# Kernel tuning notes

Hardware: AMD Instinct MI355X
Metric: run time of the kernel (lower is better)

The kernel has to match this reference:

```python
import jax, jax.numpy as jnp
import numpy as np

B, N, D, H, DFF = 2, 2048, 1024, 16, 4096
HD = D // H
L = 3
WINDOWS = (256, 64, 16)   # sliding-window size per hierarchy level
LEVEL_SCALE = 16          # pos_l = token_idx // LEVEL_SCALE**l
EPS = 1e-5
NEG = -1e9


def setup_inputs() -> dict:
    key = jax.random.key(0)
    ks = jax.random.split(key, 16)
    s = 0.02
    x = jax.random.normal(ks[0], (B, N, D), dtype=jnp.float32)
    idx = jnp.arange(N, dtype=jnp.int32)
    positions = jnp.stack([idx // (LEVEL_SCALE ** l) for l in range(L)], axis=0)  # [L, N]
    return {
        "x": x,
        "positions": positions,
        "w_qkv": jax.random.normal(ks[1], (D, 3 * D), dtype=jnp.float32) * s,
        "b_qkv": jnp.zeros((3 * D,), dtype=jnp.float32),
        "w_out": jax.random.normal(ks[2], (D, D), dtype=jnp.float32) * s,
        "b_out": jnp.zeros((D,), dtype=jnp.float32),
        "w_ff1": jax.random.normal(ks[3], (D, DFF), dtype=jnp.float32) * s,
        "b_ff1": jnp.zeros((DFF,), dtype=jnp.float32),
        "w_ff2": jax.random.normal(ks[4], (DFF, D), dtype=jnp.float32) * s,
        "b_ff2": jnp.zeros((D,), dtype=jnp.float32),
        "g1": jnp.ones((D,), dtype=jnp.float32),
        "beta1": jnp.zeros((D,), dtype=jnp.float32),
        "g2": jnp.ones((D,), dtype=jnp.float32),
        "beta2": jnp.zeros((D,), dtype=jnp.float32),
    }


def _layernorm(x, g, b):
    m = jnp.mean(x, axis=-1, keepdims=True)
    v = jnp.var(x, axis=-1, keepdims=True)
    return (x - m) * jax.lax.rsqrt(v + EPS) * g + b


def _mlswa_mask(positions):
    # union over levels of per-level sliding windows: |pos_l[i]-pos_l[j]| < w_l
    allowed = jnp.zeros((N, N), dtype=bool)
    for l, w in enumerate(WINDOWS):
        p = positions[l]
        allowed = allowed | (jnp.abs(p[:, None] - p[None, :]) < w)
    return allowed  # [N, N]


def reference(x, positions, w_qkv, b_qkv, w_out, b_out,
              w_ff1, b_ff1, w_ff2, b_ff2, g1, beta1, g2, beta2):
    residual = x
    xn = _layernorm(x, g1, beta1)
    qkv = xn @ w_qkv + b_qkv                       # [B, N, 3D]
    qkv = qkv.reshape(B, N, 3, H, HD)
    q, k, v = qkv[:, :, 0], qkv[:, :, 1], qkv[:, :, 2]  # [B, N, H, HD]

    scale = 1.0 / np.sqrt(HD)
    scores = jnp.einsum('bihd,bjhd->bhij', q, k) * scale  # [B, H, N, N]
    allowed = _mlswa_mask(positions)
    scores = jnp.where(allowed[None, None], scores, NEG)
    attn = jax.nn.softmax(scores, axis=-1)
    out = jnp.einsum('bhij,bjhd->bihd', attn, v).reshape(B, N, D)
    out = out @ w_out + b_out
    x = residual + out

    residual = x
    xn = _layernorm(x, g2, beta2)
    ff = jax.nn.gelu(xn @ w_ff1 + b_ff1, approximate=False) @ w_ff2 + b_ff2
    return residual + ff
```

## Files before the change

kernel.cpp:

```cpp
#include <hip/hip_runtime.h>
#include <cstdint>
#include <cstddef>


using u16 = unsigned short;
using u32 = unsigned int;

typedef __attribute__((ext_vector_type(8)))  short bf16x8;
typedef __attribute__((ext_vector_type(4)))  float f32x4;
typedef __attribute__((ext_vector_type(16))) float f32x16;

#define DEV __device__ __forceinline__

DEV u16 f2bf(float f) {
  u32 u = __builtin_bit_cast(u32, f);
  u32 r = (u + 0x7FFFu + ((u >> 16) & 1u)) >> 16;
  return (u16)r;
}
DEV float bf2f(u16 u) { return __builtin_bit_cast(float, (u32)u << 16); }
DEV u32 pk2(float a, float b) { return (u32)f2bf(a) | ((u32)f2bf(b) << 16); }
DEV u32 cvtpk(float lo, float hi) {
  u32 r;
  asm("v_cvt_pk_bf16_f32 %0, %1, %2" : "=v"(r) : "v"(lo), "v"(hi));
  return r;
}
DEV float fexp2(float x) { return __builtin_amdgcn_exp2f(x); }

DEV void gload_lds16(const void* g, void* lds) {
  __builtin_amdgcn_global_load_lds(
      (const __attribute__((address_space(1))) u32*)g,
      (__attribute__((address_space(3))) u32*)lds, 16, 0, 0);
}

DEV float fast_gelu(float x) {
  float u = x * fmaf(0.035677408137f, x * x, 0.7978845608f);
  u = fminf(fmaxf(u, -15.0f), 15.0f);
  float e = fexp2(u * 2.885390081777927f);
  return x * e * __builtin_amdgcn_rcpf(e + 1.0f);
}

__global__ __launch_bounds__(256) void k_transpose_bf16(const float* __restrict__ in,
                                                        u16* __restrict__ out, int R, int C) {
  __shared__ float ts[32][33];
  int n0 = blockIdx.x * 32, r0 = blockIdx.y * 32;
  int t = threadIdx.x;
  int c = t & 31, r = t >> 5;
#pragma unroll
  for (int j = 0; j < 4; ++j)
    ts[r + 8 * j][c] = in[(size_t)(r0 + r + 8 * j) * C + n0 + c];
  __syncthreads();
#pragma unroll
  for (int j = 0; j < 4; ++j)
    out[(size_t)(n0 + r + 8 * j) * R + r0 + c] = f2bf(ts[c][r + 8 * j]);
}

__global__ __launch_bounds__(256) void k_layernorm(const float* __restrict__ x,
                                                   const float* __restrict__ g,
                                                   const float* __restrict__ be,
                                                   u16* __restrict__ o) {
  int row = blockIdx.x;
  int t = threadIdx.x;
  const float* xr = x + (size_t)row * 1024;
  f32x4 v = *(const f32x4*)(xr + t * 4);
  float s = v[0] + v[1] + v[2] + v[3];
  float s2 = v[0] * v[0] + v[1] * v[1] + v[2] * v[2] + v[3] * v[3];
#pragma unroll
  for (int off = 1; off < 64; off <<= 1) {
    s += __shfl_xor(s, off);
    s2 += __shfl_xor(s2, off);
  }
  __shared__ float red[8];
  if ((t & 63) == 0) { red[t >> 6] = s; red[4 + (t >> 6)] = s2; }
  __syncthreads();
  s = red[0] + red[1] + red[2] + red[3];
  s2 = red[4] + red[5] + red[6] + red[7];
  float mean = s * (1.0f / 1024.0f);
  float var = fmaxf(s2 * (1.0f / 1024.0f) - mean * mean, 0.0f);
  float rstd = rsqrtf(var + 1e-5f);
  f32x4 gg = *(const f32x4*)(g + t * 4);
  f32x4 bb = *(const f32x4*)(be + t * 4);
  uint2 ww;
  ww.x = pk2((v[0] - mean) * rstd * gg[0] + bb[0], (v[1] - mean) * rstd * gg[1] + bb[1]);
  ww.y = pk2((v[2] - mean) * rstd * gg[2] + bb[2], (v[3] - mean) * rstd * gg[3] + bb[3]);
  *(uint2*)(o + (size_t)row * 1024 + t * 4) = ww;
}

template <int MODE, int SPLIT, int DBUF>
__global__ __launch_bounds__(SPLIT * 256) void k_gemm(
    const u16* __restrict__ A, const u16* __restrict__ Bt, int K, int NC,
    const float* __restrict__ bias, const float* __restrict__ resid,
    void* __restrict__ o0, void* __restrict__ o1, void* __restrict__ o2) {
  __shared__ u16 tiles[SPLIT][1 + DBUF][2][128 * 64];
  const int lane = threadIdx.x & 63, wave = threadIdx.x >> 6;
  const int group = (SPLIT >= 2) ? (wave >> 2) : 0;
  const int wv = wave & 3;
  const int nwg = gridDim.x * gridDim.y;
  const int id = blockIdx.y * gridDim.x + blockIdx.x;
  const int wg = (id & 7) * (nwg >> 3) + (id >> 3);
  const int tN = (wg % gridDim.x) * 128, tM = (wg / gridDim.x) * 128;
  const int wm = (wv >> 1) * 64, wn = (wv & 1) * 64;
  const int lm = lane & 15, lh = lane >> 4;
  const int K2 = K / SPLIT;
  const int kbase = group * K2;
  f32x4 acc[4][4] = {};

  auto STAGE = [&](int k0, int buf) {
#pragma unroll
    for (int i = 0; i < 4; ++i) {
      int seg = i * 4 + wv;
      int li = seg * 64 + lane;
      int m = li >> 3, ch = li & 7;
      gload_lds16(A + (size_t)(tM + m) * K + kbase + k0 + ((ch ^ (m & 7)) << 3),
                  (void*)(tiles[group][buf][0] + seg * 512));
      gload_lds16(Bt + (size_t)(tN + m) * K + kbase + k0 + ((ch ^ (m & 7)) << 3),
                  (void*)(tiles[group][buf][1] + seg * 512));
    }
  };

  auto COMPUTE = [&](int buf) {
#pragma unroll
    for (int s = 0; s < 2; ++s) {
      bf16x8 af[4], bfr[4];
#pragma unroll
      for (int i = 0; i < 4; ++i) {
        int m = wm + i * 16 + lm;
        af[i] = *(const bf16x8*)((const char*)tiles[group][buf][0] + m * 128 +
                                 (((s * 4 + lh) ^ (m & 7)) << 4));
      }
#pragma unroll
      for (int j = 0; j < 4; ++j) {
        int n = wn + j * 16 + lm;
        bfr[j] = *(const bf16x8*)((const char*)tiles[group][buf][1] + n * 128 +
                                  (((s * 4 + lh) ^ (n & 7)) << 4));
      }
#pragma unroll
      for (int i = 0; i < 4; ++i)
#pragma unroll
        for (int j = 0; j < 4; ++j)
          acc[i][j] = __builtin_amdgcn_mfma_f32_16x16x32_bf16(af[i], bfr[j], acc[i][j], 0, 0, 0);
    }
  };

  const int nk = K2 >> 6;
  if constexpr (DBUF == 1) {
    STAGE(0, 0);
    for (int t = 0; t < nk; ++t) {
      const int cur = t & 1;
      if (t + 1 < nk) {
        STAGE((t + 1) << 6, cur ^ 1);
        asm volatile("s_waitcnt vmcnt(8)" ::: "memory");
      } else {
        asm volatile("s_waitcnt vmcnt(0)" ::: "memory");
      }
      __builtin_amdgcn_s_barrier();
      COMPUTE(cur);
      __builtin_amdgcn_s_barrier();
    }
  } else {
    for (int t = 0; t < nk; ++t) {
      __syncthreads();
      STAGE(t << 6, 0);
      __syncthreads();
      COMPUTE(0);
    }
  }

  auto dumpacc = [&](float* c) {
#pragma unroll
    for (int i = 0; i < 4; ++i)
#pragma unroll
      for (int j = 0; j < 4; ++j)
        *(f32x4*)&c[(i * 4 + j) * 1024 + wv * 256 + lane * 4] = acc[i][j];
  };
  auto addacc = [&](const float* c) {
#pragma unroll
    for (int i = 0; i < 4; ++i)
#pragma unroll
      for (int j = 0; j < 4; ++j) {
        f32x4 o4 = *(const f32x4*)&c[(i * 4 + j) * 1024 + wv * 256 + lane * 4];
#pragma unroll
        for (int r = 0; r < 4; ++r) acc[i][j][r] += o4[r];
      }
  };

  if constexpr (SPLIT == 4) {
    float* cA = (float*)&tiles[0][0][0][0];
    float* cB = (float*)&tiles[2][0][0][0];
    __syncthreads();
    if (group == 1) dumpacc(cA);
    if (group == 3) dumpacc(cB);
    __syncthreads();
    if (group == 0) addacc(cA);
    if (group == 2) addacc(cB);
    __syncthreads();
    if (group == 2) dumpacc(cA);
    __syncthreads();
    if (group == 0) { addacc(cA); dumpacc(cB); }
    __syncthreads();
    {
      const int i = group;
#pragma unroll
      for (int j = 0; j < 4; ++j) {
        int gn = tN + wn + j * 16 + lm;
        int gm0 = tM + wm + i * 16 + lh * 4;
        f32x4 v4 = *(const f32x4*)&cB[(i * 4 + j) * 1024 + wv * 256 + lane * 4];
        float bv = bias[gn];
#pragma unroll
        for (int r = 0; r < 4; ++r)
          ((float*)o0)[(size_t)(gm0 + r) * NC + gn] =
              v4[r] + bv + resid[(size_t)(gm0 + r) * NC + gn];
      }
    }
    return;
  }

  if constexpr (SPLIT == 2) {
    float* comb = (float*)tiles;
    __syncthreads();
    if (group == 1) dumpacc(comb);
    __syncthreads();
    if (group == 1) return;
    addacc(comb);
  }

#pragma unroll
  for (int i = 0; i < 4; ++i) {
#pragma unroll
    for (int j = 0; j < 4; ++j) {
      int gn = tN + wn + j * 16 + lm;
      int gm0 = tM + wm + i * 16 + lh * 4;
      float vals[4];
#pragma unroll
      for (int r = 0; r < 4; ++r) vals[r] = acc[i][j][r] + bias[gn];
      if constexpr (MODE == 0) {
        int which = gn >> 10, h = (gn >> 6) & 15, d = gn & 63;
        int b = gm0 >> 11, nn0 = gm0 & 2047;
        if (which == 2) {
          uint2 w2;
          w2.x = pk2(vals[0], vals[1]);
          w2.y = pk2(vals[2], vals[3]);
          *(uint2*)((u16*)o2 + ((size_t)(b * 16 + h) * 64 + d) * 2048 + nn0) = w2;
        } else {
          u16* dst = which == 0 ? (u16*)o0 : (u16*)o1;
          float sc = which == 0 ? 0.18033688011112042f : 1.0f;
#pragma unroll
          for (int r = 0; r < 4; ++r)
            dst[(((size_t)(b * 16 + h)) * 2048 + nn0 + r) * 64 + d] = f2bf(vals[r] * sc);
        }
      } else if constexpr (MODE == 2) {
#pragma unroll
        for (int r = 0; r < 4; ++r)
          ((u16*)o0)[(size_t)(gm0 + r) * NC + gn] = f2bf(fast_gelu(vals[r]));
      } else {
#pragma unroll
        for (int r = 0; r < 4; ++r)
          ((float*)o0)[(size_t)(gm0 + r) * NC + gn] =
              vals[r] + resid[(size_t)(gm0 + r) * NC + gn];
      }
    }
  }
}

__global__ __launch_bounds__(256) void k_attn(const u16* __restrict__ q,
                                              const u16* __restrict__ k,
                                              const u16* __restrict__ vt,
                                              u16* __restrict__ o) {
  __shared__ u16 KT[2][4096];
  __shared__ u16 VT[2][4096];
  const int tid = threadIdx.x;
  const int lane = tid & 63, wave = tid >> 6;
  const int ql = lane & 31, hi = lane >> 5;
  const int id = blockIdx.y * 16 + blockIdx.x;
  const int wg = (id & 7) * 64 + (id >> 3);
  const int qb = wg & 15, bh = wg >> 4;
  const int q0 = qb * 128 + wave * 32;

  const u16* qp = q + ((size_t)bh * 2048 + q0 + ql) * 64 + hi * 8;
  bf16x8 qf[4];
#pragma unroll
  for (int dc = 0; dc < 4; ++dc) qf[dc] = *(const bf16x8*)(qp + dc * 16);

  const u16* kst = k + (size_t)bh * 2048 * 64;
  const u16* vst = vt + (size_t)bh * 64 * 2048;

  f32x16 ot0 = {0, 0, 0, 0, 0, 0, 0, 0, 0, 0, 0, 0, 0, 0, 0, 0};
  f32x16 ot1 = ot0;
  f32x16 ot2 = ot0;
  const bf16x8 ones1 = {16256, 16256, 16256, 16256, 16256, 16256, 16256, 16256};

  u32 koffA[4], koffB[4], voffA[4], voffB[4];
#pragma unroll
  for (int dc = 0; dc < 4; ++dc) {
    u32 sw = (((u32)((dc << 1) | hi) ^ (ql & 7)) << 3);
    koffA[dc] = (ql << 6) + sw;
    koffB[dc] = ((32 + ql) << 6) + sw;
  }
#pragma unroll
  for (int kc = 0; kc < 2; ++kc)
#pragma unroll
    for (int dh = 0; dh < 2; ++dh) {
      u32 rb = ((u32)((dh << 5) + ql) << 6);
      voffA[kc * 2 + dh] = rb + ((((kc << 1) + hi) ^ (ql & 7)) << 3);
      voffB[kc * 2 + dh] = rb + (((4 + (kc << 1) + hi) ^ (ql & 7)) << 3);
    }

  auto STAGE = [&](int tl, int b) {
    int kb = tl << 6;
#pragma unroll
    for (int i = 0; i < 2; ++i) {
      int seg = i * 4 + wave;
      int li = seg * 64 + lane;
      int row = li >> 3, ch = li & 7;
      int sw = (ch ^ (row & 7)) << 3;
      gload_lds16(kst + (size_t)(kb + row) * 64 + sw, (void*)&KT[b][seg * 512]);
      gload_lds16(vst + (size_t)row * 2048 + kb + sw, (void*)&VT[b][seg * 512]);
    }
  };

  auto COMPUTE = [&](const u16* KTb, const u16* VTb) {
    f32x16 st0 = {0, 0, 0, 0, 0, 0, 0, 0, 0, 0, 0, 0, 0, 0, 0, 0};
    f32x16 st1 = st0;
    bf16x8 kfa[4], kfb[4];
#pragma unroll
    for (int dc = 0; dc < 4; ++dc) {
      kfa[dc] = *(const bf16x8*)(KTb + koffA[dc]);
      kfb[dc] = *(const bf16x8*)(KTb + koffB[dc]);
    }
    __builtin_amdgcn_s_setprio(1);
#pragma unroll
    for (int dc = 0; dc < 4; ++dc) {
      st0 = __builtin_amdgcn_mfma_f32_32x32x16_bf16(kfa[dc], qf[dc], st0, 0, 0, 0);
      st1 = __builtin_amdgcn_mfma_f32_32x32x16_bf16(kfb[dc], qf[dc], st1, 0, 0, 0);
    }
    __builtin_amdgcn_s_setprio(0);
    bf16x8 vf0[4], vf1[4];
#pragma unroll
    for (int i = 0; i < 4; ++i) {
      vf0[i] = *(const bf16x8*)(VTb + voffA[i]);
      vf1[i] = *(const bf16x8*)(VTb + voffB[i]);
    }
    float p0[16], p1v[16];
#pragma unroll
    for (int r = 0; r < 16; ++r) {
      p0[r] = fexp2(st0[r]);
      p1v[r] = fexp2(st1[r]);
    }
    __builtin_amdgcn_s_setprio(1);
#pragma unroll
    for (int kc = 0; kc < 2; ++kc) {
      u32 x0 = cvtpk(p0[kc * 8 + 0], p0[kc * 8 + 1]), x1 = cvtpk(p0[kc * 8 + 2], p0[kc * 8 + 3]);
      u32 y0 = cvtpk(p0[kc * 8 + 4], p0[kc * 8 + 5]), y1 = cvtpk(p0[kc * 8 + 6], p0[kc * 8 + 7]);
      asm("v_permlane32_swap_b32 %0, %1" : "+v"(x0), "+v"(y0));
      asm("v_permlane32_swap_b32 %0, %1" : "+v"(x1), "+v"(y1));
      union { u32 u[4]; bf16x8 v8; } pf;
      pf.u[0] = x0; pf.u[1] = x1; pf.u[2] = y0; pf.u[3] = y1;
      ot0 = __builtin_amdgcn_mfma_f32_32x32x16_bf16(vf0[kc * 2 + 0], pf.v8, ot0, 0, 0, 0);
      ot1 = __builtin_amdgcn_mfma_f32_32x32x16_bf16(vf0[kc * 2 + 1], pf.v8, ot1, 0, 0, 0);
      ot2 = __builtin_amdgcn_mfma_f32_32x32x16_bf16(ones1, pf.v8, ot2, 0, 0, 0);
    }
#pragma unroll
    for (int kc = 0; kc < 2; ++kc) {
      u32 x0 = cvtpk(p1v[kc * 8 + 0], p1v[kc * 8 + 1]), x1 = cvtpk(p1v[kc * 8 + 2], p1v[kc * 8 + 3]);
      u32 y0 = cvtpk(p1v[kc * 8 + 4], p1v[kc * 8 + 5]), y1 = cvtpk(p1v[kc * 8 + 6], p1v[kc * 8 + 7]);
      asm("v_permlane32_swap_b32 %0, %1" : "+v"(x0), "+v"(y0));
      asm("v_permlane32_swap_b32 %0, %1" : "+v"(x1), "+v"(y1));
      union { u32 u[4]; bf16x8 v8; } pf;
      pf.u[0] = x0; pf.u[1] = x1; pf.u[2] = y0; pf.u[3] = y1;
      ot0 = __builtin_amdgcn_mfma_f32_32x32x16_bf16(vf1[kc * 2 + 0], pf.v8, ot0, 0, 0, 0);
      ot1 = __builtin_amdgcn_mfma_f32_32x32x16_bf16(vf1[kc * 2 + 1], pf.v8, ot1, 0, 0, 0);
      ot2 = __builtin_amdgcn_mfma_f32_32x32x16_bf16(ones1, pf.v8, ot2, 0, 0, 0);
    }
    __builtin_amdgcn_s_setprio(0);
  };

  STAGE(0, 0);
  __syncthreads();

#pragma unroll 1
  for (int t2 = 0; t2 < 16; ++t2) {
    const int tlA = t2 * 2;
    STAGE(tlA + 1, 1);
    COMPUTE(KT[0], VT[0]);
    __syncthreads();
    if (t2 < 15) STAGE(tlA + 2, 0);
    COMPUTE(KT[1], VT[1]);
    __syncthreads();
  }

  float inv = 1.0f / ot2[0];
  int b = bh >> 4, h = bh & 15;
  size_t ob = ((size_t)b * 2048 + q0 + ql) * 1024 + h * 64;
#pragma unroll
  for (int r = 0; r < 16; ++r) {
    int d = (r & 3) + ((r >> 2) << 3) + hi * 4;
    o[ob + d] = f2bf(ot0[r] * inv);
    o[ob + 32 + d] = f2bf(ot1[r] * inv);
  }
}

extern "C" void kernel_launch(void* const* d_in, const int* in_sizes, int n_in,
                              void* d_out, int out_size, void* d_ws, size_t ws_size,
                              hipStream_t stream) {
  const float* x = (const float*)d_in[0];
  const float* w_qkv = (const float*)d_in[2];
  const float* b_qkv = (const float*)d_in[3];
  const float* w_out = (const float*)d_in[4];
  const float* b_out = (const float*)d_in[5];
  const float* w_ff1 = (const float*)d_in[6];
  const float* b_ff1 = (const float*)d_in[7];
  const float* w_ff2 = (const float*)d_in[8];
  const float* b_ff2 = (const float*)d_in[9];
  const float* g1 = (const float*)d_in[10];
  const float* be1 = (const float*)d_in[11];
  const float* g2 = (const float*)d_in[12];
  const float* be2 = (const float*)d_in[13];
  float* out = (float*)d_out;

  char* wp = (char*)d_ws;
  u16* wqkvT = (u16*)wp; wp += (size_t)3072 * 1024 * 2;
  u16* woutT = (u16*)wp; wp += (size_t)1024 * 1024 * 2;
  u16* wff1T = (u16*)wp; wp += (size_t)4096 * 1024 * 2;
  u16* wff2T = (u16*)wp; wp += (size_t)1024 * 4096 * 2;
  u16* xn    = (u16*)wp; wp += (size_t)4096 * 1024 * 2;
  float* x2  = (float*)wp; wp += (size_t)4096 * 1024 * 4;
  u16* qbuf  = (u16*)wp; wp += (size_t)32 * 2048 * 64 * 2;
  u16* kbuf  = (u16*)wp; wp += (size_t)32 * 2048 * 64 * 2;
  u16* vtbuf = (u16*)wp; wp += (size_t)32 * 2048 * 64 * 2;
  u16* attnb = (u16*)wp; wp += (size_t)4096 * 1024 * 2;
  u16* ffh   = qbuf;

  k_transpose_bf16<<<dim3(3072 / 32, 1024 / 32), 256, 0, stream>>>(w_qkv, wqkvT, 1024, 3072);
  k_transpose_bf16<<<dim3(1024 / 32, 1024 / 32), 256, 0, stream>>>(w_out, woutT, 1024, 1024);
  k_transpose_bf16<<<dim3(4096 / 32, 1024 / 32), 256, 0, stream>>>(w_ff1, wff1T, 1024, 4096);
  k_transpose_bf16<<<dim3(1024 / 32, 4096 / 32), 256, 0, stream>>>(w_ff2, wff2T, 4096, 1024);

  k_layernorm<<<4096, 256, 0, stream>>>(x, g1, be1, xn);
  k_gemm<0, 2, 0><<<dim3(24, 32), 512, 0, stream>>>(xn, wqkvT, 1024, 3072, b_qkv, nullptr,
                                                    qbuf, kbuf, vtbuf);
  k_attn<<<dim3(16, 32), 256, 0, stream>>>(qbuf, kbuf, vtbuf, attnb);
  k_gemm<1, 2, 1><<<dim3(8, 32), 512, 0, stream>>>(attnb, woutT, 1024, 1024, b_out, x,
                                                   x2, nullptr, nullptr);
  k_layernorm<<<4096, 256, 0, stream>>>(x2, g2, be2, xn);
  k_gemm<2, 2, 0><<<dim3(32, 32), 512, 0, stream>>>(xn, wff1T, 1024, 4096, b_ff1, nullptr,
                                                    ffh, nullptr, nullptr);
  k_gemm<3, 2, 1><<<dim3(8, 32), 512, 0, stream>>>(ffh, wff2T, 4096, 1024, b_ff2, x2,
                                                   out, nullptr, nullptr);
}
```

Measured before the change: 231.0 us.

## Deepen attention K/V staging to four LDS buffers with explicit vmcnt waits

Measured after the change: 230.1 us. About the same (-0.4%).

```diff
diff --git a/kernel.cpp b/kernel.cpp
--- a/kernel.cpp
+++ b/kernel.cpp
@@ -183,37 +183,6 @@
       }
   };
 
-  if constexpr (SPLIT == 4) {
-    float* cA = (float*)&tiles[0][0][0][0];
-    float* cB = (float*)&tiles[2][0][0][0];
-    __syncthreads();
-    if (group == 1) dumpacc(cA);
-    if (group == 3) dumpacc(cB);
-    __syncthreads();
-    if (group == 0) addacc(cA);
-    if (group == 2) addacc(cB);
-    __syncthreads();
-    if (group == 2) dumpacc(cA);
-    __syncthreads();
-    if (group == 0) { addacc(cA); dumpacc(cB); }
-    __syncthreads();
-    {
-      const int i = group;
-#pragma unroll
-      for (int j = 0; j < 4; ++j) {
-        int gn = tN + wn + j * 16 + lm;
-        int gm0 = tM + wm + i * 16 + lh * 4;
-        f32x4 v4 = *(const f32x4*)&cB[(i * 4 + j) * 1024 + wv * 256 + lane * 4];
-        float bv = bias[gn];
-#pragma unroll
-        for (int r = 0; r < 4; ++r)
-          ((float*)o0)[(size_t)(gm0 + r) * NC + gn] =
-              v4[r] + bv + resid[(size_t)(gm0 + r) * NC + gn];
-      }
-    }
-    return;
-  }
-
   if constexpr (SPLIT == 2) {
     float* comb = (float*)tiles;
     __syncthreads();
@@ -265,8 +234,8 @@
                                               const u16* __restrict__ k,
                                               const u16* __restrict__ vt,
                                               u16* __restrict__ o) {
-  __shared__ u16 KT[2][4096];
-  __shared__ u16 VT[2][4096];
+  __shared__ u16 KT[4][4096];
+  __shared__ u16 VT[4][4096];
   const int tid = threadIdx.x;
   const int lane = tid & 63, wave = tid >> 6;
   const int ql = lane & 31, hi = lane >> 5;
@@ -374,17 +343,21 @@
   };
 
   STAGE(0, 0);
-  __syncthreads();
-
+  STAGE(1, 1);
 #pragma unroll 1
   for (int t2 = 0; t2 < 16; ++t2) {
-    const int tlA = t2 * 2;
-    STAGE(tlA + 1, 1);
-    COMPUTE(KT[0], VT[0]);
-    __syncthreads();
-    if (t2 < 15) STAGE(tlA + 2, 0);
-    COMPUTE(KT[1], VT[1]);
-    __syncthreads();
+    const int pa = (t2 & 1) << 1;
+    if (t2 < 15) {
+      STAGE(2 * t2 + 2, pa ^ 2);
+      STAGE(2 * t2 + 3, (pa ^ 2) | 1);
+      asm volatile("s_waitcnt vmcnt(8)" ::: "memory");
+    } else {
+      asm volatile("s_waitcnt vmcnt(0)" ::: "memory");
+    }
+    __builtin_amdgcn_s_barrier();
+    COMPUTE(KT[pa], VT[pa]);
+    COMPUTE(KT[pa | 1], VT[pa | 1]);
+    __builtin_amdgcn_s_barrier();
   }
 
   float inv = 1.0f / ot2[0];
```
